# Kernel tuning notes

Hardware: AMD Instinct MI355X
Metric: run time of the kernel (lower is better)

Reference implementation:

```python
import jax, jax.numpy as jnp
import numpy as np


def _ln(x, g, b):
    m = x.mean(-1, keepdims=True)
    v = ((x - m) ** 2).mean(-1, keepdims=True)
    return (x - m) * jax.lax.rsqrt(v + 1e-5) * g + b


def _forward(x, fx_in, pre_w1, pre_b1, pre_w2, pre_b2, placeholder,
             ln1_g, ln1_b, px_w, px_b, pfx_w, pfx_b, slice_w, slice_b, temp,
             q_w, k_w, v_w, out_w, out_b, ln2_g, ln2_b,
             mlp_w1, mlp_b1, mlp_w2, mlp_b2,
             ln3_g, ln3_b, head_w1, head_b1, head_w2, head_b2):
    # All linear weights are stored as [in, out] (pre-transposed vs torch nn.Linear).
    B, N, _ = x.shape
    L, H = temp.shape
    dh = slice_w.shape[1]
    gelu = lambda t: jax.nn.gelu(t, approximate=False)
    # preprocess MLP (n_layers=0, res=False): Linear -> GELU -> Linear
    h = jnp.concatenate([x, fx_in], axis=-1)
    h = gelu(h @ pre_w1 + pre_b1) @ pre_w2 + pre_b2
    h = h + placeholder  # learned [D] offset
    scale = 1.0 / jnp.sqrt(jnp.asarray(dh, h.dtype))
    for i in range(L):  # loop over structurally distinct layers
        y = _ln(h, ln1_g[i], ln1_b[i])
        # project to per-head features: bhnd
        fx_mid = (y @ pfx_w[i] + pfx_b[i]).reshape(B, N, H, dh).transpose(0, 2, 1, 3)
        x_mid = (y @ px_w[i] + px_b[i]).reshape(B, N, H, dh).transpose(0, 2, 1, 3)
        # soft slice assignment over G slices
        logits = jnp.einsum('bhnd,dg->bhng', x_mid, slice_w[i]) + slice_b[i]
        sw = jax.nn.softmax(logits / temp[i][None, :, None, None], axis=-1)  # bhng
        norm = sw.sum(axis=2)  # bhg
        tok = jnp.einsum('bhnd,bhng->bhgd', fx_mid, sw) / (norm + 1e-5)[..., None]
        # attention over G=slice_num tokens
        q = tok @ q_w[i]
        k = tok @ k_w[i]
        v = tok @ v_w[i]
        attn = jax.nn.softmax(jnp.einsum('bhgd,bhmd->bhgm', q, k) * scale, axis=-1)
        out_slice = jnp.einsum('bhgm,bhmd->bhgd', attn, v)
        # deslice back to points
        out_x = jnp.einsum('bhgd,bhng->bhnd', out_slice, sw)
        out_x = out_x.transpose(0, 2, 1, 3).reshape(B, N, H * dh)
        h = h + (out_x @ out_w[i] + out_b[i])
        z = _ln(h, ln2_g[i], ln2_b[i])
        h = h + (gelu(z @ mlp_w1[i] + mlp_b1[i]) @ mlp_w2[i] + mlp_b2[i])
    z = _ln(h, ln3_g, ln3_b)
    return gelu(z @ head_w1 + head_b1) @ head_w2 + head_b2


def setup_inputs() -> dict:
    key = jax.random.key(0)
    B, N, D, H, dh, G, L = 2, 16384, 256, 8, 32, 64, 5
    SP, FUN, OUT = 2, 4, 4
    ID = H * dh  # inner_dim == n_hidden
    MR = D * 1   # mlp_ratio=1
    ks = iter(jax.random.split(key, 64))
    nrm = lambda shape, s=0.02: jax.random.normal(next(ks), shape, jnp.float32) * s
    return dict(
        x=jax.random.normal(next(ks), (B, N, SP), jnp.float32),
        fx_in=jax.random.normal(next(ks), (B, N, FUN), jnp.float32),
        pre_w1=nrm((SP + FUN, 2 * D)), pre_b1=jnp.zeros((2 * D,), jnp.float32),
        pre_w2=nrm((2 * D, D)), pre_b2=jnp.zeros((D,), jnp.float32),
        placeholder=nrm((D,)),
        ln1_g=jnp.ones((L, D), jnp.float32), ln1_b=jnp.zeros((L, D), jnp.float32),
        px_w=nrm((L, D, ID)), px_b=jnp.zeros((L, ID), jnp.float32),
        pfx_w=nrm((L, D, ID)), pfx_b=jnp.zeros((L, ID), jnp.float32),
        slice_w=nrm((L, dh, G), 0.1), slice_b=jnp.zeros((L, G), jnp.float32),
        temp=0.5 * jnp.ones((L, H), jnp.float32),
        q_w=nrm((L, dh, dh), 0.1), k_w=nrm((L, dh, dh), 0.1), v_w=nrm((L, dh, dh), 0.1),
        out_w=nrm((L, ID, D)), out_b=jnp.zeros((L, D), jnp.float32),
        ln2_g=jnp.ones((L, D), jnp.float32), ln2_b=jnp.zeros((L, D), jnp.float32),
        mlp_w1=nrm((L, D, MR)), mlp_b1=jnp.zeros((L, MR), jnp.float32),
        mlp_w2=nrm((L, MR, D)), mlp_b2=jnp.zeros((L, D), jnp.float32),
        ln3_g=jnp.ones((D,), jnp.float32), ln3_b=jnp.zeros((D,), jnp.float32),
        head_w1=nrm((D, D)), head_b1=jnp.zeros((D,), jnp.float32),
        head_w2=nrm((D, OUT)), head_b2=jnp.zeros((OUT,), jnp.float32),
    )


def reference(x, fx_in, pre_w1, pre_b1, pre_w2, pre_b2, placeholder,
              ln1_g, ln1_b, px_w, px_b, pfx_w, pfx_b, slice_w, slice_b, temp,
              q_w, k_w, v_w, out_w, out_b, ln2_g, ln2_b,
              mlp_w1, mlp_b1, mlp_w2, mlp_b2,
              ln3_g, ln3_b, head_w1, head_b1, head_w2, head_b2):
    return _forward(x, fx_in, pre_w1, pre_b1, pre_w2, pre_b2, placeholder,
                    ln1_g, ln1_b, px_w, px_b, pfx_w, pfx_b, slice_w, slice_b, temp,
                    q_w, k_w, v_w, out_w, out_b, ln2_g, ln2_b,
                    mlp_w1, mlp_b1, mlp_w2, mlp_b2,
                    ln3_g, ln3_b, head_w1, head_b1, head_w2, head_b2)
```

## Files before the change

kernel.cpp:

```cpp
#include <hip/hip_runtime.h>


#define MTOK 32768
#define NB   16384

typedef unsigned short u16;
using short8 = __attribute__((ext_vector_type(8))) short;
using f4     = __attribute__((ext_vector_type(4))) float;

__device__ __forceinline__ float bfu(u16 u) {
    return __uint_as_float(((unsigned)u) << 16);
}
__device__ __forceinline__ u16 f2bf(float f) {
    unsigned u = __float_as_uint(f);
    u += 0x7FFFu + ((u >> 16) & 1u);
    return (u16)(u >> 16);
}
__device__ __forceinline__ float ldf(const void* p, int i, int isbf) {
    return isbf ? bfu(((const u16*)p)[i]) : ((const float*)p)[i];
}
__device__ __forceinline__ float4 dec4(ushort4 u) {
    return make_float4(bfu(u.x), bfu(u.y), bfu(u.z), bfu(u.w));
}
__device__ __forceinline__ float gelu_f(float x) {
    return 0.5f * x * (1.0f + erff(x * 0.7071067811865475f));
}

typedef __attribute__((address_space(1))) const unsigned int* as1p;
typedef __attribute__((address_space(3))) unsigned int* as3p;
__device__ __forceinline__ void gload_lds16(const u16* g, u16* l) {
    __builtin_amdgcn_global_load_lds((as1p)g, (as3p)l, 16, 0, 0);
}

#define F_H      ((size_t)0)
#define F_OS     ((size_t)8388608)
#define F_TOKP   ((size_t)8421376)
#define F_NORMP  ((size_t)10518528)
#define F_TOK    ((size_t)10584064)
#define F_NORM   ((size_t)10616832)
#define F_BIAS   ((size_t)10617856)
#define F_PARAMS ((size_t)10626048)
#define F_BF     ((size_t)10858884)
#define B_PB2C 0
#define B_OUTB 256
#define B_M1B  1536
#define B_M2B  2816
#define B_HB1  4096
#define B_SP   4352
#define B_END  8192
#define U_WT     ((size_t)0)
#define WT_PRE2  0
#define WT_HEAD1 131072
#define WT_SPFX  196608
#define WT_OUT   1179648
#define WT_MLP1  1507328
#define WT_MLP2  1835008
#define WT_END   2162688
#define U_Y   ((size_t)2162688)
#define U_XM  ((size_t)10551296)
#define U_FM  ((size_t)18939904)
#define U_SW  ((size_t)27328512)

#define P_X    0
#define P_FX   65536
#define P_W1   196608
#define P_B1   199680
#define P_LN1G 200192
#define P_LN1B 201472
#define P_LN2G 202752
#define P_LN2B 204032
#define P_LN3G 205312
#define P_LN3B 205568
#define P_SLW  205824
#define P_SLB  216064
#define P_TEMP 216384
#define P_QW   216448
#define P_KW   221568
#define P_VW   226688
#define P_HW2  231808
#define P_HB2  232832
#define P_END  232836

__global__ __launch_bounds__(256) void cvt_kernel(
    const void* x, const void* fx, const void* w1, const void* b1,
    const void* l1g, const void* l1b, const void* l2g, const void* l2b,
    const void* l3g, const void* l3b, const void* slw, const void* slb,
    const void* tmp, const void* qw, const void* kw, const void* vw,
    const void* hw2, const void* hb2, float* __restrict__ P)
{
    int isbf = (((const u16*)tmp)[0] != 0);
    int idx = blockIdx.x * 256 + threadIdx.x;
    const void* s; int o;
    if      (idx < 65536)  { s = x;   o = idx; }
    else if (idx < 196608) { s = fx;  o = idx - 65536; }
    else if (idx < 199680) { s = w1;  o = idx - 196608; }
    else if (idx < 200192) { s = b1;  o = idx - 199680; }
    else if (idx < 201472) { s = l1g; o = idx - 200192; }
    else if (idx < 202752) { s = l1b; o = idx - 201472; }
    else if (idx < 204032) { s = l2g; o = idx - 202752; }
    else if (idx < 205312) { s = l2b; o = idx - 204032; }
    else if (idx < 205568) { s = l3g; o = idx - 205312; }
    else if (idx < 205824) { s = l3b; o = idx - 205568; }
    else if (idx < 216064) { s = slw; o = idx - 205824; }
    else if (idx < 216384) { s = slb; o = idx - 216064; }
    else if (idx < 216424) { s = tmp; o = idx - 216384; }
    else if (idx < 216448) { return; }
    else if (idx < 221568) { s = qw;  o = idx - 216448; }
    else if (idx < 226688) { s = kw;  o = idx - 221568; }
    else if (idx < 231808) { s = vw;  o = idx - 226688; }
    else if (idx < 232832) { s = hw2; o = idx - 231808; }
    else if (idx < 232836) { s = hb2; o = idx - 232832; }
    else return;
    P[idx] = ldf(s, o, isbf);
}

__global__ __launch_bounds__(256) void prep_main(
    const void* pre_w2, const void* head_w1, const void* pfx_w,
    const void* out_w, const void* mlp_w1, const void* mlp_w2,
    const void* pre_b2, const void* placeholder, const void* pfx_b,
    const void* out_b, const void* mlp_b1, const void* mlp_b2,
    const void* head_b1, const void* tmp,
    u16* __restrict__ WT, float* __restrict__ BIAS)
{
    int isbf = (((const u16*)tmp)[0] != 0);
    int idx = blockIdx.x * 256 + threadIdx.x;
    if (idx < 131072) {
        int n = idx >> 9, k = idx & 511;
        WT[WT_PRE2 + idx] = f2bf(ldf(pre_w2, k * 256 + n, isbf));
    } else if (idx < 196608) {
        int f = idx - 131072;
        int n = f >> 8, k = f & 255;
        WT[WT_HEAD1 + f] = f2bf(ldf(head_w1, k * 256 + n, isbf));
    } else if (idx < 524288) {
        int f = idx - 196608;
        int i = f >> 16, r = f & 65535;
        int n = r >> 8, k = r & 255;
        WT[WT_SPFX + (size_t)i * 196608 + (512 + n) * 256 + k] =
            f2bf(ldf(pfx_w, i * 65536 + k * 256 + n, isbf));
    } else if (idx < 1507328) {
        int f = idx - 524288;
        int mat = f >> 16, r = f & 65535;
        const void* s; int off = (mat % 5) * 65536;
        if      (mat < 5)  s = out_w;
        else if (mat < 10) s = mlp_w1;
        else               s = mlp_w2;
        int n = r >> 8, k = r & 255;
        WT[WT_OUT + f] = f2bf(ldf(s, off + k * 256 + n, isbf));
    } else if (idx < 1507584) {
        int c = idx - 1507328;
        BIAS[B_PB2C + c] = ldf(pre_b2, c, isbf) + ldf(placeholder, c, isbf);
    } else if (idx < 1508864) {
        int o = idx - 1507584; BIAS[B_OUTB + o] = ldf(out_b, o, isbf);
    } else if (idx < 1510144) {
        int o = idx - 1508864; BIAS[B_M1B + o] = ldf(mlp_b1, o, isbf);
    } else if (idx < 1511424) {
        int o = idx - 1510144; BIAS[B_M2B + o] = ldf(mlp_b2, o, isbf);
    } else if (idx < 1511680) {
        int o = idx - 1511424; BIAS[B_HB1 + o] = ldf(head_b1, o, isbf);
    } else if (idx < 1512960) {
        int o = idx - 1511680;
        int i = o >> 8, c = o & 255;
        BIAS[B_SP + i * 768 + 512 + c] = ldf(pfx_b, o, isbf);
    }
}

__global__ __launch_bounds__(256) void prep_pxsl(
    const void* px_w, const void* px_b, const void* slw, const void* slb,
    const void* tmp, u16* __restrict__ WT, float* __restrict__ BIAS)
{
    int isbf = (((const u16*)tmp)[0] != 0);
    __shared__ float pxs[64 * 33];
    __shared__ float sls[2048];
    int blk = blockIdx.x;
    int i = blk >> 5, h = (blk >> 2) & 7, kb = blk & 3;
    int t = threadIdx.x;
#pragma unroll
    for (int p = 0; p < 8; ++p) {
        int flat = t + 256 * p;
        sls[flat] = ldf(slw, i * 2048 + flat, isbf);
        int k = flat >> 5, d = flat & 31;
        pxs[k * 33 + d] = ldf(px_w, i * 65536 + (kb * 64 + k) * 256 + h * 32 + d, isbf);
    }
    __syncthreads();
    int k = t & 63, gb = t >> 6;
    float acc[16];
#pragma unroll
    for (int gi = 0; gi < 16; ++gi) acc[gi] = 0.f;
#pragma unroll
    for (int d = 0; d < 32; ++d) {
        float pv = pxs[k * 33 + d];
        const float* sp = sls + d * 64 + gb * 16;
#pragma unroll
        for (int gi = 0; gi < 16; ++gi) acc[gi] = fmaf(pv, sp[gi], acc[gi]);
    }
    u16* WTp = WT + WT_SPFX + (size_t)i * 196608;
#pragma unroll
    for (int gi = 0; gi < 16; ++gi) {
        int n = h * 64 + gb * 16 + gi;
        WTp[n * 256 + kb * 64 + k] = f2bf(acc[gi]);
    }
    if (kb == 0 && t < 64) {
        int g = t;
        float a = ldf(slb, i * 64 + g, isbf);
#pragma unroll
        for (int d = 0; d < 32; ++d)
            a = fmaf(ldf(px_b, i * 256 + h * 32 + d, isbf), sls[d * 64 + g], a);
        BIAS[B_SP + i * 768 + h * 64 + g] = a;
    }
}

__global__ __launch_bounds__(256) void pre1_kernel(
    const float* __restrict__ P, u16* __restrict__ HID)
{
    __shared__ float w1s[3072];
    __shared__ float b1s[512];
    int t = threadIdx.x;
#pragma unroll
    for (int p = 0; p < 12; ++p) w1s[t + 256 * p] = P[P_W1 + t + 256 * p];
    b1s[t] = P[P_B1 + t];
    b1s[t + 256] = P[P_B1 + t + 256];
    __syncthreads();
    int m = blockIdx.x * 4 + (t >> 6);
    int lane = t & 63;
    float xa = P[P_X + m * 2],      xb = P[P_X + m * 2 + 1];
    float fa = P[P_FX + m * 4],     fb = P[P_FX + m * 4 + 1];
    float fc = P[P_FX + m * 4 + 2], fd = P[P_FX + m * 4 + 3];
    size_t base = (size_t)m * 512 + lane;
#pragma unroll
    for (int jj = 0; jj < 8; ++jj) {
        int j = lane + 64 * jj;
        float a = b1s[j];
        a = fmaf(xa, w1s[j], a);
        a = fmaf(xb, w1s[512 + j], a);
        a = fmaf(fa, w1s[1024 + j], a);
        a = fmaf(fb, w1s[1536 + j], a);
        a = fmaf(fc, w1s[2048 + j], a);
        a = fmaf(fd, w1s[2560 + j], a);
        HID[base + 64 * jj] = f2bf(gelu_f(a));
    }
}

template <int KK, bool RES>
__global__ __launch_bounds__(256, 2) void gemm_ln(
    const u16* __restrict__ A, const u16* __restrict__ Wt,
    const float* __restrict__ bias, const float* __restrict__ lng,
    const float* __restrict__ lnb, u16* __restrict__ Hb, u16* __restrict__ Y)
{
    __shared__ u16 As[128 * 64];
    __shared__ u16 Bs[256 * 64];
    __shared__ float rs2[2][128], rq2[2][128];
    const int t = threadIdx.x;
    const int wave = t >> 6, lane = t & 63;
    const int quad = lane >> 4, l15 = lane & 15;
    const int m0 = blockIdx.x * 128;
    const int wm = (wave & 1) * 64, wn = (wave >> 1) * 128;
    const int lrow = lane >> 3, ls = lane & 7;
    f4 acc[4][8];
#pragma unroll
    for (int i = 0; i < 4; ++i)
#pragma unroll
        for (int j = 0; j < 8; ++j) acc[i][j] = (f4){0.f, 0.f, 0.f, 0.f};

    for (int kc = 0; kc < KK; kc += 64) {
        if (kc) __syncthreads();
#pragma unroll
        for (int q = 0; q < 12; ++q) {
            int gr = wave * 96 + q * 8;
            if (gr < 128) {
                int row = gr + lrow;
                int chunk = ls ^ (row & 7);
                gload_lds16(A + (size_t)(m0 + row) * KK + kc + chunk * 8,
                            As + gr * 64);
            } else {
                int brow = gr - 128 + lrow;
                int chunk = ls ^ (brow & 7);
                gload_lds16(Wt + (size_t)brow * KK + kc + chunk * 8,
                            Bs + (gr - 128) * 64);
            }
        }
        __syncthreads();
#pragma unroll
        for (int kk = 0; kk < 2; ++kk) {
            short8 a[4], b[8];
#pragma unroll
            for (int i = 0; i < 4; ++i) {
                int R = wm + i * 16 + l15;
                a[i] = *(const short8*)(As + R * 64 + (((quad + kk * 4) ^ (R & 7)) << 3));
            }
#pragma unroll
            for (int j = 0; j < 8; ++j) {
                int Rb = wn + j * 16 + l15;
                b[j] = *(const short8*)(Bs + Rb * 64 + (((quad + kk * 4) ^ (Rb & 7)) << 3));
            }
#pragma unroll
            for (int i = 0; i < 4; ++i)
#pragma unroll
                for (int j = 0; j < 8; ++j)
                    acc[i][j] = __builtin_amdgcn_mfma_f32_16x16x32_bf16(
                        a[i], b[j], acc[i][j], 0, 0, 0);
        }
    }
    int colj[8];
    float bj[8];
#pragma unroll
    for (int j = 0; j < 8; ++j) { colj[j] = wn + j * 16 + l15; bj[j] = bias[colj[j]]; }
    const int half = wn >> 7;
#pragma unroll
    for (int i = 0; i < 4; ++i) {
#pragma unroll
        for (int r = 0; r < 4; ++r) {
            int row = wm + i * 16 + quad * 4 + r;
            size_t gbase = (size_t)(m0 + row) * 256;
            float s = 0.f, q2 = 0.f;
#pragma unroll
            for (int j = 0; j < 8; ++j) {
                float v = acc[i][j][r] + bj[j];
                if (RES) v += bfu(Hb[gbase + colj[j]]);
                Hb[gbase + colj[j]] = f2bf(v);
                acc[i][j][r] = v;
                s += v; q2 += v * v;
            }
#pragma unroll
            for (int o = 1; o < 16; o <<= 1) { s += __shfl_xor(s, o); q2 += __shfl_xor(q2, o); }
            if (l15 == 0) { rs2[half][row] = s; rq2[half][row] = q2; }
        }
    }
    __syncthreads();
    float gj[8], betj[8];
#pragma unroll
    for (int j = 0; j < 8; ++j) { gj[j] = lng[colj[j]]; betj[j] = lnb[colj[j]]; }
#pragma unroll
    for (int i = 0; i < 4; ++i) {
#pragma unroll
        for (int r = 0; r < 4; ++r) {
            int row = wm + i * 16 + quad * 4 + r;
            size_t gbase = (size_t)(m0 + row) * 256;
            float mean = (rs2[0][row] + rs2[1][row]) * (1.0f / 256.0f);
            float var = (rq2[0][row] + rq2[1][row]) * (1.0f / 256.0f) - mean * mean;
            float rstd = rsqrtf(var + 1e-5f);
#pragma unroll
            for (int j = 0; j < 8; ++j) {
                float y = (acc[i][j][r] - mean) * rstd * gj[j] + betj[j];
                Y[gbase + colj[j]] = f2bf(y);
            }
        }
    }
}

__global__ __launch_bounds__(256, 4) void gemm_gelu(
    const u16* __restrict__ A, const u16* __restrict__ Wt,
    const float* __restrict__ bias, u16* __restrict__ Cb)
{
    __shared__ u16 As[128 * 64];
    __shared__ u16 Bs[128 * 64];
    const int t = threadIdx.x;
    const int wave = t >> 6, lane = t & 63;
    const int quad = lane >> 4, l15 = lane & 15;
    const int m0 = blockIdx.x * 128;
    const int n0 = blockIdx.y * 128;
    const int wm = (wave & 1) * 64, wn = (wave >> 1) * 64;
    const int r0 = wave * 32;
    const int lrow = lane >> 3, ls = lane & 7;
    f4 acc[4][4];
#pragma unroll
    for (int i = 0; i < 4; ++i)
#pragma unroll
        for (int j = 0; j < 4; ++j) acc[i][j] = (f4){0.f, 0.f, 0.f, 0.f};

    for (int kc = 0; kc < 256; kc += 64) {
        if (kc) __syncthreads();
#pragma unroll
        for (int q = 0; q < 4; ++q) {
            int row = r0 + q * 8 + lrow;
            int chunk = ls ^ (row & 7);
            gload_lds16(A  + (size_t)(m0 + row) * 256 + kc + chunk * 8,
                        As + (r0 + q * 8) * 64);
            gload_lds16(Wt + (size_t)(n0 + row) * 256 + kc + chunk * 8,
                        Bs + (r0 + q * 8) * 64);
        }
        __syncthreads();
#pragma unroll
        for (int kk = 0; kk < 2; ++kk) {
            short8 a[4], b[4];
#pragma unroll
            for (int i = 0; i < 4; ++i) {
                int R = wm + i * 16 + l15;
                a[i] = *(const short8*)(As + R * 64 + (((quad + kk * 4) ^ (R & 7)) << 3));
            }
#pragma unroll
            for (int j = 0; j < 4; ++j) {
                int R = wn + j * 16 + l15;
                b[j] = *(const short8*)(Bs + R * 64 + (((quad + kk * 4) ^ (R & 7)) << 3));
            }
#pragma unroll
            for (int i = 0; i < 4; ++i)
#pragma unroll
                for (int j = 0; j < 4; ++j)
                    acc[i][j] = __builtin_amdgcn_mfma_f32_16x16x32_bf16(
                        a[i], b[j], acc[i][j], 0, 0, 0);
        }
    }
#pragma unroll
    for (int j = 0; j < 4; ++j) {
        int cj = n0 + wn + j * 16 + l15;
        float bj = bias[cj];
#pragma unroll
        for (int i = 0; i < 4; ++i) {
            int rbase = m0 + wm + i * 16 + quad * 4;
#pragma unroll
            for (int r = 0; r < 4; ++r) {
                float v = gelu_f(acc[i][j][r] + bj);
                Cb[(size_t)(rbase + r) * 256 + cj] = f2bf(v);
            }
        }
    }
}

__global__ __launch_bounds__(256, 4) void gemm_spfx(
    const u16* __restrict__ A, const u16* __restrict__ Wt,
    const float* __restrict__ bsp, const float* __restrict__ tempv,
    u16* __restrict__ SW, u16* __restrict__ FM)
{
    __shared__ u16 As[128 * 64];
    __shared__ u16 Bs[128 * 64];
    const int t = threadIdx.x;
    const int wave = t >> 6, lane = t & 63;
    const int quad = lane >> 4, l15 = lane & 15;
    const int m0 = blockIdx.x * 128;
    const int n0 = blockIdx.y * 128;
    const int wm = (wave & 1) * 64, wn = (wave >> 1) * 64;
    const int r0 = wave * 32;
    const int lrow = lane >> 3, ls = lane & 7;
    f4 acc[4][4];
#pragma unroll
    for (int i = 0; i < 4; ++i)
#pragma unroll
        for (int j = 0; j < 4; ++j) acc[i][j] = (f4){0.f, 0.f, 0.f, 0.f};

    for (int kc = 0; kc < 256; kc += 64) {
        if (kc) __syncthreads();
#pragma unroll
        for (int q = 0; q < 4; ++q) {
            int row = r0 + q * 8 + lrow;
            int chunk = ls ^ (row & 7);
            gload_lds16(A  + (size_t)(m0 + row) * 256 + kc + chunk * 8,
                        As + (r0 + q * 8) * 64);
            gload_lds16(Wt + (size_t)(n0 + row) * 256 + kc + chunk * 8,
                        Bs + (r0 + q * 8) * 64);
        }
        __syncthreads();
#pragma unroll
        for (int kk = 0; kk < 2; ++kk) {
            short8 a[4], b[4];
#pragma unroll
            for (int i = 0; i < 4; ++i) {
                int R = wm + i * 16 + l15;
                a[i] = *(const short8*)(As + R * 64 + (((quad + kk * 4) ^ (R & 7)) << 3));
            }
#pragma unroll
            for (int j = 0; j < 4; ++j) {
                int R = wn + j * 16 + l15;
                b[j] = *(const short8*)(Bs + R * 64 + (((quad + kk * 4) ^ (R & 7)) << 3));
            }
#pragma unroll
            for (int i = 0; i < 4; ++i)
#pragma unroll
                for (int j = 0; j < 4; ++j)
                    acc[i][j] = __builtin_amdgcn_mfma_f32_16x16x32_bf16(
                        a[i], b[j], acc[i][j], 0, 0, 0);
        }
    }
    float bj[4];
#pragma unroll
    for (int j = 0; j < 4; ++j) bj[j] = bsp[n0 + wn + j * 16 + l15];
    if (blockIdx.y < 4) {
        const int h = (n0 + wn) >> 6;
        const float itemp = 1.0f / tempv[h];
#pragma unroll
        for (int i = 0; i < 4; ++i) {
#pragma unroll
            for (int r = 0; r < 4; ++r) {
                float v[4];
                float mx = -3.0e38f;
#pragma unroll
                for (int j = 0; j < 4; ++j) {
                    v[j] = (acc[i][j][r] + bj[j]) * itemp;
                    mx = fmaxf(mx, v[j]);
                }
#pragma unroll
                for (int o = 1; o < 16; o <<= 1) mx = fmaxf(mx, __shfl_xor(mx, o));
                float s = 0.f;
#pragma unroll
                for (int j = 0; j < 4; ++j) { v[j] = expf(v[j] - mx); s += v[j]; }
#pragma unroll
                for (int o = 1; o < 16; o <<= 1) s += __shfl_xor(s, o);
                float inv = 1.0f / s;
                int m = m0 + wm + i * 16 + quad * 4 + r;
                int b = m >> 14, n = m & 16383;
                size_t base = (((size_t)(b * 8 + h)) * NB + n) * 64;
#pragma unroll
                for (int j = 0; j < 4; ++j)
                    SW[base + j * 16 + l15] = f2bf(v[j] * inv);
            }
        }
    } else {
        int cj = (n0 - 512) + wn + l15;
#pragma unroll
        for (int j = 0; j < 4; ++j) {
            int col = cj + j * 16;
#pragma unroll
            for (int i = 0; i < 4; ++i) {
                int rbase = m0 + wm + i * 16 + quad * 4;
#pragma unroll
                for (int r = 0; r < 4; ++r)
                    FM[(size_t)(rbase + r) * 256 + col] = f2bf(acc[i][j][r] + bj[j]);
            }
        }
    }
}

__global__ __launch_bounds__(256) void tok1_kernel(
    const u16* __restrict__ FM, const u16* __restrict__ SW,
    float* __restrict__ TOKP, float* __restrict__ NORMP)
{
    int bh = blockIdx.x >> 6, chunk = blockIdx.x & 63;
    int b = bh >> 3, hd = bh & 7;
    int t = threadIdx.x, wave = t >> 6, lane = t & 63;
    int g0 = (lane >> 3) * 8, d0 = (lane & 7) * 4;
    float4 acc[8];
#pragma unroll
    for (int gi = 0; gi < 8; ++gi) acc[gi] = make_float4(0.f, 0.f, 0.f, 0.f);
    float4 n0a = make_float4(0.f, 0.f, 0.f, 0.f);
    float4 n1a = make_float4(0.f, 0.f, 0.f, 0.f);
    int nbase = chunk * 256 + wave * 64;
    const u16* fmB = FM + ((size_t)b * NB + nbase) * 256 + hd * 32 + d0;
    const u16* swB = SW + ((size_t)bh * NB + nbase) * 64 + g0;
    for (int j = 0; j < 64; ++j) {
        float4 f4v = dec4(*(const ushort4*)(fmB + (size_t)j * 256));
        float4 s0 = dec4(*(const ushort4*)(swB + (size_t)j * 64));
        float4 s1 = dec4(*(const ushort4*)(swB + (size_t)j * 64 + 4));
#define TOKACC(gi, sv)                                            \
        acc[gi].x = fmaf(f4v.x, sv, acc[gi].x);                   \
        acc[gi].y = fmaf(f4v.y, sv, acc[gi].y);                   \
        acc[gi].z = fmaf(f4v.z, sv, acc[gi].z);                   \
        acc[gi].w = fmaf(f4v.w, sv, acc[gi].w);
        TOKACC(0, s0.x) TOKACC(1, s0.y) TOKACC(2, s0.z) TOKACC(3, s0.w)
        TOKACC(4, s1.x) TOKACC(5, s1.y) TOKACC(6, s1.z) TOKACC(7, s1.w)
#undef TOKACC
        n0a.x += s0.x; n0a.y += s0.y; n0a.z += s0.z; n0a.w += s0.w;
        n1a.x += s1.x; n1a.y += s1.y; n1a.z += s1.z; n1a.w += s1.w;
    }
    __shared__ float red[4][2048];
    __shared__ float nred[4][64];
#pragma unroll
    for (int gi = 0; gi < 8; ++gi)
        *(float4*)&red[wave][(g0 + gi) * 32 + d0] = acc[gi];
    if ((lane & 7) == 0) {
        nred[wave][g0 + 0] = n0a.x; nred[wave][g0 + 1] = n0a.y;
        nred[wave][g0 + 2] = n0a.z; nred[wave][g0 + 3] = n0a.w;
        nred[wave][g0 + 4] = n1a.x; nred[wave][g0 + 5] = n1a.y;
        nred[wave][g0 + 6] = n1a.z; nred[wave][g0 + 7] = n1a.w;
    }
    __syncthreads();
    size_t tokBase = (size_t)(chunk * 16 + bh) * 2048;
#pragma unroll
    for (int k = 0; k < 8; ++k) {
        int c = t + 256 * k;
        TOKP[tokBase + c] = red[0][c] + red[1][c] + red[2][c] + red[3][c];
    }
    if (t < 64)
        NORMP[(chunk * 16 + bh) * 64 + t] = nred[0][t] + nred[1][t] + nred[2][t] + nred[3][t];
}

__global__ __launch_bounds__(256) void tok2_kernel(
    const float* __restrict__ TOKP, const float* __restrict__ NORMP,
    float* __restrict__ TOK, float* __restrict__ NORM)
{
    int idx = blockIdx.x * 256 + threadIdx.x;
    if (idx < 32768) {
        int bh = idx >> 11, c = idx & 2047;
        float s = 0.f;
#pragma unroll 8
        for (int ch = 0; ch < 64; ++ch) s += TOKP[(size_t)(ch * 16 + bh) * 2048 + c];
        TOK[idx] = s;
    } else if (idx < 33792) {
        int o = idx - 32768;
        int bh = o >> 6, g = o & 63;
        float s = 0.f;
#pragma unroll 8
        for (int ch = 0; ch < 64; ++ch) s += NORMP[(ch * 16 + bh) * 64 + g];
        NORM[o] = s;
    }
}

__global__ __launch_bounds__(256) void attn_kernel(
    const float* __restrict__ TOK, const float* __restrict__ NORM,
    const float* __restrict__ qw, const float* __restrict__ kw,
    const float* __restrict__ vw, float* __restrict__ OS)
{
    __shared__ float tokd[2048], qs[2048], ks[2048], vs[2048];
    int bh = blockIdx.x;
    int t = threadIdx.x;
#pragma unroll
    for (int i = 0; i < 2; ++i) {
        int f4v = t + 256 * i;
        float4 v = *(const float4*)(TOK + (size_t)bh * 2048 + f4v * 4);
        float inv = 1.0f / (NORM[bh * 64 + (f4v >> 3)] + 1e-5f);
        v.x *= inv; v.y *= inv; v.z *= inv; v.w *= inv;
        *(float4*)&tokd[f4v * 4] = v;
    }
    __syncthreads();
#pragma unroll
    for (int i = 0; i < 8; ++i) {
        int f = t + 256 * i;
        int g = f >> 5, d = f & 31;
        const float* tr = tokd + g * 32;
        float aq = 0.f, ak = 0.f, av = 0.f;
#pragma unroll
        for (int e = 0; e < 32; ++e) {
            float tv = tr[e];
            aq = fmaf(tv, qw[e * 32 + d], aq);
            ak = fmaf(tv, kw[e * 32 + d], ak);
            av = fmaf(tv, vw[e * 32 + d], av);
        }
        qs[f] = aq; ks[f] = ak; vs[f] = av;
    }
    __syncthreads();
    int g = t >> 2, sub = t & 3;
    float4 qv[8];
#pragma unroll
    for (int e4 = 0; e4 < 8; ++e4) qv[e4] = *(const float4*)(qs + g * 32 + e4 * 4);
    float p[16];
    float mx = -3.0e38f;
#pragma unroll
    for (int mm = 0; mm < 16; ++mm) {
        int mI = sub * 16 + mm;
        const float4* kr = (const float4*)(ks + mI * 32);
        float s = 0.f;
#pragma unroll
        for (int e4 = 0; e4 < 8; ++e4) {
            float4 kv = kr[e4];
            s = fmaf(qv[e4].x, kv.x, s); s = fmaf(qv[e4].y, kv.y, s);
            s = fmaf(qv[e4].z, kv.z, s); s = fmaf(qv[e4].w, kv.w, s);
        }
        s *= 0.17677669529663687f;
        p[mm] = s;
        mx = fmaxf(mx, s);
    }
    mx = fmaxf(mx, __shfl_xor(mx, 1));
    mx = fmaxf(mx, __shfl_xor(mx, 2));
    float lsum = 0.f;
#pragma unroll
    for (int mm = 0; mm < 16; ++mm) { p[mm] = expf(p[mm] - mx); lsum += p[mm]; }
    lsum += __shfl_xor(lsum, 1);
    lsum += __shfl_xor(lsum, 2);
    float inv = 1.0f / lsum;
    float4 oa[8];
#pragma unroll
    for (int d4 = 0; d4 < 8; ++d4) oa[d4] = make_float4(0.f, 0.f, 0.f, 0.f);
#pragma unroll
    for (int mm = 0; mm < 16; ++mm) {
        int mI = sub * 16 + mm;
        const float4* vr = (const float4*)(vs + mI * 32);
        float pm = p[mm];
#pragma unroll
        for (int d4 = 0; d4 < 8; ++d4) {
            float4 vv = vr[d4];
            oa[d4].x = fmaf(pm, vv.x, oa[d4].x);
            oa[d4].y = fmaf(pm, vv.y, oa[d4].y);
            oa[d4].z = fmaf(pm, vv.z, oa[d4].z);
            oa[d4].w = fmaf(pm, vv.w, oa[d4].w);
        }
    }
#pragma unroll
    for (int d4 = 0; d4 < 8; ++d4) {
        oa[d4].x += __shfl_xor(oa[d4].x, 1); oa[d4].x += __shfl_xor(oa[d4].x, 2);
        oa[d4].y += __shfl_xor(oa[d4].y, 1); oa[d4].y += __shfl_xor(oa[d4].y, 2);
        oa[d4].z += __shfl_xor(oa[d4].z, 1); oa[d4].z += __shfl_xor(oa[d4].z, 2);
        oa[d4].w += __shfl_xor(oa[d4].w, 1); oa[d4].w += __shfl_xor(oa[d4].w, 2);
    }
    float4 r0 = oa[sub * 2], r1 = oa[sub * 2 + 1];
    r0.x *= inv; r0.y *= inv; r0.z *= inv; r0.w *= inv;
    r1.x *= inv; r1.y *= inv; r1.z *= inv; r1.w *= inv;
    *(float4*)(OS + (size_t)bh * 2048 + g * 32 + sub * 8)     = r0;
    *(float4*)(OS + (size_t)bh * 2048 + g * 32 + sub * 8 + 4) = r1;
}

__global__ __launch_bounds__(256) void deslice_kernel(
    const float* __restrict__ OS, const u16* __restrict__ SW, u16* __restrict__ OX)
{
    __shared__ float swt[8 * 16 * 64];
    int blk = blockIdx.x;
    int b = blk >> 10, n0 = (blk & 1023) * 16;
    int t = threadIdx.x;
    int hd = t >> 5, d = t & 31;
#pragma unroll
    for (int i = 0; i < 8; ++i) {
        int f4v = t + 256 * i;
        int hd2 = f4v >> 8, mm = (f4v >> 4) & 15, g4 = f4v & 15;
        ushort4 u = *(const ushort4*)(SW + (((size_t)(b * 8 + hd2)) * NB + n0 + mm) * 64 + g4 * 4);
        *(float4*)&swt[(hd2 * 16 + mm) * 64 + g4 * 4] = dec4(u);
    }
    __syncthreads();
    float acc[16];
#pragma unroll
    for (int mm = 0; mm < 16; ++mm) acc[mm] = 0.f;
    const float* osb = OS + ((size_t)(b * 8 + hd)) * 2048 + d;
#pragma unroll 4
    for (int g4 = 0; g4 < 16; ++g4) {
        float o0 = osb[(g4 * 4 + 0) * 32], o1 = osb[(g4 * 4 + 1) * 32];
        float o2 = osb[(g4 * 4 + 2) * 32], o3 = osb[(g4 * 4 + 3) * 32];
        const float* swp = swt + hd * 1024 + g4 * 4;
#pragma unroll
        for (int mm = 0; mm < 16; ++mm) {
            float4 sv = *(const float4*)(swp + mm * 64);
            acc[mm] = fmaf(o0, sv.x, fmaf(o1, sv.y, fmaf(o2, sv.z, fmaf(o3, sv.w, acc[mm]))));
        }
    }
#pragma unroll
    for (int mm = 0; mm < 16; ++mm)
        OX[((size_t)b * NB + n0 + mm) * 256 + t] = f2bf(acc[mm]);
}

__global__ __launch_bounds__(256) void head2_kernel(
    const u16* __restrict__ HID, const float* __restrict__ w2,
    const float* __restrict__ b2, const void* tmp, void* __restrict__ OUT)
{
    int isbf = (((const u16*)tmp)[0] != 0);
    int lane = threadIdx.x & 63;
    size_t m = (size_t)blockIdx.x * 4 + (threadIdx.x >> 6);
    const float4 hv = dec4(*(const ushort4*)(HID + m * 256 + lane * 4));
    float4 a = make_float4(0.f, 0.f, 0.f, 0.f);
    float hcomp[4] = {hv.x, hv.y, hv.z, hv.w};
#pragma unroll
    for (int i = 0; i < 4; ++i) {
        const float4 wv = *(const float4*)(w2 + (lane * 4 + i) * 4);
        float h = hcomp[i];
        a.x = fmaf(h, wv.x, a.x); a.y = fmaf(h, wv.y, a.y);
        a.z = fmaf(h, wv.z, a.z); a.w = fmaf(h, wv.w, a.w);
    }
#pragma unroll
    for (int o = 32; o; o >>= 1) {
        a.x += __shfl_xor(a.x, o); a.y += __shfl_xor(a.y, o);
        a.z += __shfl_xor(a.z, o); a.w += __shfl_xor(a.w, o);
    }
    if (lane == 0) {
        float o0 = a.x + b2[0], o1 = a.y + b2[1], o2 = a.z + b2[2], o3 = a.w + b2[3];
        if (isbf) {
            ushort4 r; r.x = f2bf(o0); r.y = f2bf(o1); r.z = f2bf(o2); r.w = f2bf(o3);
            *(ushort4*)((u16*)OUT + m * 4) = r;
        } else {
            *(float4*)((float*)OUT + m * 4) = make_float4(o0, o1, o2, o3);
        }
    }
}

extern "C" void kernel_launch(void* const* d_in, const int* in_sizes, int n_in,
                              void* d_out, int out_size, void* d_ws, size_t ws_size,
                              hipStream_t stream)
{
    const void* x = d_in[0];      const void* fx = d_in[1];
    const void* pre_w1 = d_in[2]; const void* pre_b1 = d_in[3];
    const void* pre_w2 = d_in[4]; const void* pre_b2 = d_in[5];
    const void* placeholder = d_in[6];
    const void* ln1_g = d_in[7];  const void* ln1_b = d_in[8];
    const void* px_w = d_in[9];   const void* px_b = d_in[10];
    const void* pfx_w = d_in[11]; const void* pfx_b = d_in[12];
    const void* slice_w = d_in[13]; const void* slice_b = d_in[14];
    const void* temp = d_in[15];
    const void* q_w = d_in[16];   const void* k_w = d_in[17]; const void* v_w = d_in[18];
    const void* out_w = d_in[19]; const void* out_b = d_in[20];
    const void* ln2_g = d_in[21]; const void* ln2_b = d_in[22];
    const void* mlp_w1 = d_in[23]; const void* mlp_b1 = d_in[24];
    const void* mlp_w2 = d_in[25]; const void* mlp_b2 = d_in[26];
    const void* ln3_g = d_in[27]; const void* ln3_b = d_in[28];
    const void* head_w1 = d_in[29]; const void* head_b1 = d_in[30];
    const void* head_w2 = d_in[31]; const void* head_b2 = d_in[32];

    float* ws = (float*)d_ws;
    u16*   Hb    = (u16*)(ws + F_H);
    float* OSp   = ws + F_OS;
    float* TOKP  = ws + F_TOKP;
    float* NORMP = ws + F_NORMP;
    float* TOKf  = ws + F_TOK;
    float* NORMf = ws + F_NORM;
    float* BIAS  = ws + F_BIAS;
    float* P     = ws + F_PARAMS;
    u16*   U     = (u16*)(ws + F_BF);
    u16*   WT    = U + U_WT;
    u16*   Yb    = U + U_Y;
    u16*   XMb   = U + U_XM;
    u16*   FMb   = U + U_FM;
    u16*   SWb   = U + U_SW;
    u16*   HIDb  = U + U_XM;

    cvt_kernel<<<910, 256, 0, stream>>>(x, fx, pre_w1, pre_b1, ln1_g, ln1_b,
        ln2_g, ln2_b, ln3_g, ln3_b, slice_w, slice_b, temp, q_w, k_w, v_w,
        head_w2, head_b2, P);
    prep_main<<<5910, 256, 0, stream>>>(pre_w2, head_w1, pfx_w, out_w, mlp_w1,
        mlp_w2, pre_b2, placeholder, pfx_b, out_b, mlp_b1, mlp_b2, head_b1,
        temp, WT, BIAS);
    prep_pxsl<<<160, 256, 0, stream>>>(px_w, px_b, slice_w, slice_b, temp, WT, BIAS);
    pre1_kernel<<<8192, 256, 0, stream>>>(P, HIDb);

    dim3 gpl(256, 2);
    dim3 gsp(256, 6);
    gemm_ln<512, false><<<256, 256, 0, stream>>>(HIDb, WT + WT_PRE2,
        BIAS + B_PB2C, P + P_LN1G, P + P_LN1B, Hb, Yb);

    for (int i = 0; i < 5; ++i) {
        gemm_spfx<<<gsp, 256, 0, stream>>>(Yb, WT + WT_SPFX + (size_t)i * 196608,
            BIAS + B_SP + i * 768, P + P_TEMP + i * 8, SWb, FMb);
        tok1_kernel<<<1024, 256, 0, stream>>>(FMb, SWb, TOKP, NORMP);
        tok2_kernel<<<132, 256, 0, stream>>>(TOKP, NORMP, TOKf, NORMf);
        attn_kernel<<<16, 256, 0, stream>>>(TOKf, NORMf, P + P_QW + i * 1024,
            P + P_KW + i * 1024, P + P_VW + i * 1024, OSp);
        deslice_kernel<<<2048, 256, 0, stream>>>(OSp, SWb, Yb);
        gemm_ln<256, true><<<256, 256, 0, stream>>>(Yb, WT + WT_OUT + i * 65536,
            BIAS + B_OUTB + i * 256, P + P_LN2G + i * 256, P + P_LN2B + i * 256, Hb, Yb);
        gemm_gelu<<<gpl, 256, 0, stream>>>(Yb, WT + WT_MLP1 + i * 65536,
            BIAS + B_M1B + i * 256, XMb);
        const float* ng = (i < 4) ? (P + P_LN1G + (i + 1) * 256) : (P + P_LN3G);
        const float* nb = (i < 4) ? (P + P_LN1B + (i + 1) * 256) : (P + P_LN3B);
        gemm_ln<256, true><<<256, 256, 0, stream>>>(XMb, WT + WT_MLP2 + i * 65536,
            BIAS + B_M2B + i * 256, ng, nb, Hb, Yb);
    }

    gemm_gelu<<<gpl, 256, 0, stream>>>(Yb, WT + WT_HEAD1, BIAS + B_HB1, XMb);
    head2_kernel<<<8192, 256, 0, stream>>>(XMb, P + P_HW2, P + P_HB2, temp, d_out);
}
```

Measured before the change: 1.138 ms.

## Halve gemm_ln row tile and transpose weights through shared-memory tiles

The fused GEMM+LayerNorm kernel now uses 64-row tiles instead of 128, doubling the grid to 512 blocks and raising launch bounds to 3 blocks per SM. With MTOK 32768, the old 256-block grid roughly matches the 256 CUs on MI355X, so this is meant to improve occupancy and latency hiding, at the cost of loading the weight tile for twice as many blocks. Separately, the weight-prep kernel now transposes through 64x64 LDS tiles so global reads and writes are coalesced, replacing strided per-element reads. That prep work is one-time setup and a small part of the total.

```diff
diff --git a/kernel.cpp b/kernel.cpp
--- a/kernel.cpp
+++ b/kernel.cpp
@@ -123,44 +123,61 @@
     u16* __restrict__ WT, float* __restrict__ BIAS)
 {
     int isbf = (((const u16*)tmp)[0] != 0);
-    int idx = blockIdx.x * 256 + threadIdx.x;
-    if (idx < 131072) {
-        int n = idx >> 9, k = idx & 511;
-        WT[WT_PRE2 + idx] = f2bf(ldf(pre_w2, k * 256 + n, isbf));
-    } else if (idx < 196608) {
-        int f = idx - 131072;
-        int n = f >> 8, k = f & 255;
-        WT[WT_HEAD1 + f] = f2bf(ldf(head_w1, k * 256 + n, isbf));
-    } else if (idx < 524288) {
-        int f = idx - 196608;
-        int i = f >> 16, r = f & 65535;
-        int n = r >> 8, k = r & 255;
-        WT[WT_SPFX + (size_t)i * 196608 + (512 + n) * 256 + k] =
-            f2bf(ldf(pfx_w, i * 65536 + k * 256 + n, isbf));
-    } else if (idx < 1507328) {
-        int f = idx - 524288;
-        int mat = f >> 16, r = f & 65535;
-        const void* s; int off = (mat % 5) * 65536;
-        if      (mat < 5)  s = out_w;
-        else if (mat < 10) s = mlp_w1;
-        else               s = mlp_w2;
-        int n = r >> 8, k = r & 255;
-        WT[WT_OUT + f] = f2bf(ldf(s, off + k * 256 + n, isbf));
-    } else if (idx < 1507584) {
-        int c = idx - 1507328;
-        BIAS[B_PB2C + c] = ldf(pre_b2, c, isbf) + ldf(placeholder, c, isbf);
-    } else if (idx < 1508864) {
-        int o = idx - 1507584; BIAS[B_OUTB + o] = ldf(out_b, o, isbf);
-    } else if (idx < 1510144) {
-        int o = idx - 1508864; BIAS[B_M1B + o] = ldf(mlp_b1, o, isbf);
-    } else if (idx < 1511424) {
-        int o = idx - 1510144; BIAS[B_M2B + o] = ldf(mlp_b2, o, isbf);
-    } else if (idx < 1511680) {
-        int o = idx - 1511424; BIAS[B_HB1 + o] = ldf(head_b1, o, isbf);
-    } else if (idx < 1512960) {
-        int o = idx - 1511680;
-        int i = o >> 8, c = o & 255;
-        BIAS[B_SP + i * 768 + 512 + c] = ldf(pfx_b, o, isbf);
+    int blk = blockIdx.x;
+    int t = threadIdx.x;
+    if (blk < 368) {
+        __shared__ float tile[64][65];
+        const void* src; size_t srcoff; size_t dbase; int dstride;
+        int k0, n0;
+        if (blk < 32) {
+            int tk = blk >> 2, tn = blk & 3;
+            src = pre_w2; srcoff = 0;
+            k0 = tk * 64; n0 = tn * 64;
+            dbase = WT_PRE2; dstride = 512;
+        } else {
+            int m = (blk - 32) >> 4, tl = (blk - 32) & 15;
+            int tk = tl >> 2, tn = tl & 3;
+            k0 = tk * 64; n0 = tn * 64; dstride = 256;
+            if (m == 0)       { src = head_w1; srcoff = 0;               dbase = WT_HEAD1; }
+            else if (m <= 5)  { int i = m - 1;  src = pfx_w;  srcoff = (size_t)i * 65536;
+                                dbase = WT_SPFX + (size_t)i * 196608 + (size_t)512 * 256; }
+            else if (m <= 10) { int i = m - 6;  src = out_w;  srcoff = (size_t)i * 65536;
+                                dbase = WT_OUT + (size_t)i * 65536; }
+            else if (m <= 15) { int i = m - 11; src = mlp_w1; srcoff = (size_t)i * 65536;
+                                dbase = WT_MLP1 + (size_t)i * 65536; }
+            else              { int i = m - 16; src = mlp_w2; srcoff = (size_t)i * 65536;
+                                dbase = WT_MLP2 + (size_t)i * 65536; }
+        }
+#pragma unroll
+        for (int p = 0; p < 16; ++p) {
+            int flat = t + 256 * p;
+            int r = flat >> 6, c = flat & 63;
+            tile[r][c] = ldf(src, srcoff + (size_t)(k0 + r) * 256 + n0 + c, isbf);
+        }
+        __syncthreads();
+#pragma unroll
+        for (int p = 0; p < 16; ++p) {
+            int flat = t + 256 * p;
+            int r = flat >> 6, c = flat & 63;
+            WT[dbase + (size_t)(n0 + r) * dstride + k0 + c] = f2bf(tile[c][r]);
+        }
+    } else {
+        int idx = (blk - 368) * 256 + t;
+        if (idx < 256) {
+            BIAS[B_PB2C + idx] = ldf(pre_b2, idx, isbf) + ldf(placeholder, idx, isbf);
+        } else if (idx < 1536) {
+            int o = idx - 256;  BIAS[B_OUTB + o] = ldf(out_b, o, isbf);
+        } else if (idx < 2816) {
+            int o = idx - 1536; BIAS[B_M1B + o] = ldf(mlp_b1, o, isbf);
+        } else if (idx < 4096) {
+            int o = idx - 2816; BIAS[B_M2B + o] = ldf(mlp_b2, o, isbf);
+        } else if (idx < 4352) {
+            int o = idx - 4096; BIAS[B_HB1 + o] = ldf(head_b1, o, isbf);
+        } else if (idx < 5632) {
+            int o = idx - 4352;
+            int i = o >> 8, c = o & 255;
+            BIAS[B_SP + i * 768 + 512 + c] = ldf(pfx_b, o, isbf);
+        }
     }
 }
 
@@ -241,49 +258,49 @@
 }
 
 template <int KK, bool RES>
-__global__ __launch_bounds__(256, 2) void gemm_ln(
+__global__ __launch_bounds__(256, 3) void gemm_ln(
     const u16* __restrict__ A, const u16* __restrict__ Wt,
     const float* __restrict__ bias, const float* __restrict__ lng,
     const float* __restrict__ lnb, u16* __restrict__ Hb, u16* __restrict__ Y)
 {
-    __shared__ u16 As[128 * 64];
+    __shared__ u16 As[64 * 64];
     __shared__ u16 Bs[256 * 64];
-    __shared__ float rs2[2][128], rq2[2][128];
+    __shared__ float rs2[2][64], rq2[2][64];
     const int t = threadIdx.x;
     const int wave = t >> 6, lane = t & 63;
     const int quad = lane >> 4, l15 = lane & 15;
-    const int m0 = blockIdx.x * 128;
-    const int wm = (wave & 1) * 64, wn = (wave >> 1) * 128;
+    const int m0 = blockIdx.x * 64;
+    const int wm = (wave & 1) * 32, wn = (wave >> 1) * 128;
     const int lrow = lane >> 3, ls = lane & 7;
-    f4 acc[4][8];
-#pragma unroll
-    for (int i = 0; i < 4; ++i)
+    f4 acc[2][8];
+#pragma unroll
+    for (int i = 0; i < 2; ++i)
 #pragma unroll
         for (int j = 0; j < 8; ++j) acc[i][j] = (f4){0.f, 0.f, 0.f, 0.f};
 
     for (int kc = 0; kc < KK; kc += 64) {
         if (kc) __syncthreads();
 #pragma unroll
-        for (int q = 0; q < 12; ++q) {
-            int gr = wave * 96 + q * 8;
-            if (gr < 128) {
+        for (int q = 0; q < 10; ++q) {
+            int gr = wave * 80 + q * 8;
+            if (gr < 64) {
                 int row = gr + lrow;
-                int chunk = ls ^ (row & 7);
+                int chunk = ls ^ lrow;
                 gload_lds16(A + (size_t)(m0 + row) * KK + kc + chunk * 8,
                             As + gr * 64);
             } else {
-                int brow = gr - 128 + lrow;
-                int chunk = ls ^ (brow & 7);
+                int brow = gr - 64 + lrow;
+                int chunk = ls ^ lrow;
                 gload_lds16(Wt + (size_t)brow * KK + kc + chunk * 8,
-                            Bs + (gr - 128) * 64);
+                            Bs + (gr - 64) * 64);
             }
         }
         __syncthreads();
 #pragma unroll
         for (int kk = 0; kk < 2; ++kk) {
-            short8 a[4], b[8];
-#pragma unroll
-            for (int i = 0; i < 4; ++i) {
+            short8 a[2], b[8];
+#pragma unroll
+            for (int i = 0; i < 2; ++i) {
                 int R = wm + i * 16 + l15;
                 a[i] = *(const short8*)(As + R * 64 + (((quad + kk * 4) ^ (R & 7)) << 3));
             }
@@ -293,7 +310,7 @@
                 b[j] = *(const short8*)(Bs + Rb * 64 + (((quad + kk * 4) ^ (Rb & 7)) << 3));
             }
 #pragma unroll
-            for (int i = 0; i < 4; ++i)
+            for (int i = 0; i < 2; ++i)
 #pragma unroll
                 for (int j = 0; j < 8; ++j)
                     acc[i][j] = __builtin_amdgcn_mfma_f32_16x16x32_bf16(
@@ -306,7 +323,7 @@
     for (int j = 0; j < 8; ++j) { colj[j] = wn + j * 16 + l15; bj[j] = bias[colj[j]]; }
     const int half = wn >> 7;
 #pragma unroll
-    for (int i = 0; i < 4; ++i) {
+    for (int i = 0; i < 2; ++i) {
 #pragma unroll
         for (int r = 0; r < 4; ++r) {
             int row = wm + i * 16 + quad * 4 + r;
@@ -330,7 +347,7 @@
 #pragma unroll
     for (int j = 0; j < 8; ++j) { gj[j] = lng[colj[j]]; betj[j] = lnb[colj[j]]; }
 #pragma unroll
-    for (int i = 0; i < 4; ++i) {
+    for (int i = 0; i < 2; ++i) {
 #pragma unroll
         for (int r = 0; r < 4; ++r) {
             int row = wm + i * 16 + quad * 4 + r;
@@ -797,7 +814,7 @@
     cvt_kernel<<<910, 256, 0, stream>>>(x, fx, pre_w1, pre_b1, ln1_g, ln1_b,
         ln2_g, ln2_b, ln3_g, ln3_b, slice_w, slice_b, temp, q_w, k_w, v_w,
         head_w2, head_b2, P);
-    prep_main<<<5910, 256, 0, stream>>>(pre_w2, head_w1, pfx_w, out_w, mlp_w1,
+    prep_main<<<390, 256, 0, stream>>>(pre_w2, head_w1, pfx_w, out_w, mlp_w1,
         mlp_w2, pre_b2, placeholder, pfx_b, out_b, mlp_b1, mlp_b2, head_b1,
         temp, WT, BIAS);
     prep_pxsl<<<160, 256, 0, stream>>>(px_w, px_b, slice_w, slice_b, temp, WT, BIAS);
@@ -805,7 +822,7 @@
 
     dim3 gpl(256, 2);
     dim3 gsp(256, 6);
-    gemm_ln<512, false><<<256, 256, 0, stream>>>(HIDb, WT + WT_PRE2,
+    gemm_ln<512, false><<<512, 256, 0, stream>>>(HIDb, WT + WT_PRE2,
         BIAS + B_PB2C, P + P_LN1G, P + P_LN1B, Hb, Yb);
 
     for (int i = 0; i < 5; ++i) {
@@ -816,13 +833,13 @@
         attn_kernel<<<16, 256, 0, stream>>>(TOKf, NORMf, P + P_QW + i * 1024,
             P + P_KW + i * 1024, P + P_VW + i * 1024, OSp);
         deslice_kernel<<<2048, 256, 0, stream>>>(OSp, SWb, Yb);
-        gemm_ln<256, true><<<256, 256, 0, stream>>>(Yb, WT + WT_OUT + i * 65536,
+        gemm_ln<256, true><<<512, 256, 0, stream>>>(Yb, WT + WT_OUT + i * 65536,
             BIAS + B_OUTB + i * 256, P + P_LN2G + i * 256, P + P_LN2B + i * 256, Hb, Yb);
         gemm_gelu<<<gpl, 256, 0, stream>>>(Yb, WT + WT_MLP1 + i * 65536,
             BIAS + B_M1B + i * 256, XMb);
         const float* ng = (i < 4) ? (P + P_LN1G + (i + 1) * 256) : (P + P_LN3G);
         const float* nb = (i < 4) ? (P + P_LN1B + (i + 1) * 256) : (P + P_LN3B);
-        gemm_ln<256, true><<<256, 256, 0, stream>>>(XMb, WT + WT_MLP2 + i * 65536,
+        gemm_ln<256, true><<<512, 256, 0, stream>>>(XMb, WT + WT_MLP2 + i * 65536,
             BIAS + B_M2B + i * 256, ng, nb, Hb, Yb);
     }
 
```

Measured after the change: 1.113 ms. -2.2%, faster.
